# Performance work log

Measured on AMD Instinct MI355X. Metric: run time of the kernel, lower is better.

## Reference

```python
import jax, jax.numpy as jnp
import numpy as np

RADIUS = 0.8
NSAMPLE = 32
EPS = 1e-5  # BatchNorm eps


def _bn(x, gamma, beta, axes):
    # BatchNorm (training-mode batch statistics), channel dim kept via broadcasting
    m = jnp.mean(x, axis=axes, keepdims=True)
    v = jnp.var(x, axis=axes, keepdims=True)
    return (x - m) * jax.lax.rsqrt(v + EPS) * gamma + beta


def setup_inputs() -> dict:
    key = jax.random.key(0)
    ks = jax.random.split(key, 6)
    B, N, P, C, COUT = 4, 8192, 2048, 128, 256
    ffps_xyz = jax.random.uniform(ks[0], (B, P, 3), dtype=jnp.float32) * 2.0 - 1.0
    backbone_xyz = jax.random.uniform(ks[1], (B, N, 3), dtype=jnp.float32) * 2.0 - 1.0
    backbone_features = jax.random.normal(ks[2], (B, C, N), dtype=jnp.float32)
    w_shift = jax.random.normal(ks[3], (3, 3), dtype=jnp.float32) * 0.1
    gamma_shift = jnp.ones((3,), jnp.float32)
    beta_shift = jnp.zeros((3,), jnp.float32)
    w_mlp = jax.random.normal(ks[4], (COUT, 3 + C), dtype=jnp.float32) * 0.05
    gamma_mlp = jnp.ones((COUT,), jnp.float32)
    beta_mlp = jnp.zeros((COUT,), jnp.float32)
    return {
        "ffps_xyz": ffps_xyz,
        "backbone_xyz": backbone_xyz,
        "backbone_features": backbone_features,
        "w_shift": w_shift,
        "gamma_shift": gamma_shift,
        "beta_shift": beta_shift,
        "w_mlp": w_mlp,
        "gamma_mlp": gamma_mlp,
        "beta_mlp": beta_mlp,
    }


def reference(ffps_xyz, backbone_xyz, backbone_features,
              w_shift, gamma_shift, beta_shift,
              w_mlp, gamma_mlp, beta_mlp):
    B, P, _ = ffps_xyz.shape
    N = backbone_xyz.shape[1]

    # ---- shift_layer: Conv1d(3->3, k=1, no bias) + BN1d + ReLU on (B,3,P) ----
    x = jnp.einsum('oc,bpc->bop', w_shift, ffps_xyz)                  # (B,3,P)
    x = _bn(x, gamma_shift[None, :, None], beta_shift[None, :, None], (0, 2))
    new_xyz = jax.nn.relu(x).transpose(0, 2, 1)                       # (B,P,3) query centers

    # ---- QueryAndGroup: ball query (radius, nsample), use_xyz=True ----
    d2 = jnp.sum((new_xyz[:, :, None, :] - backbone_xyz[:, None, :, :]) ** 2, -1)  # (B,P,N)
    within = d2 < (RADIUS * RADIUS)
    # pick the first NSAMPLE in-radius indices (CUDA ball_query semantics)
    keyv = jnp.where(within, jnp.arange(N, dtype=jnp.int32), jnp.int32(N))
    negk, idx = jax.lax.top_k(-keyv, NSAMPLE)                          # smallest keys first
    valid = (-negk) < N
    idx = jnp.where(valid, idx, idx[..., :1])                          # pad with first found idx

    g_xyz = jnp.take_along_axis(backbone_xyz[:, None, :, :], idx[..., None], axis=2)
    g_xyz = g_xyz - new_xyz[:, :, None, :]                             # (B,P,S,3) recentered
    feats = backbone_features.transpose(0, 2, 1)                       # (B,N,C)
    g_f = jnp.take_along_axis(feats[:, None, :, :], idx[..., None], axis=2)  # (B,P,S,C)
    g = jnp.concatenate([g_xyz, g_f], axis=-1)                         # (B,P,S,3+C)

    # ---- mlp: 1x1 conv (3+C -> COUT, no bias) + BN + ReLU ----
    y = jnp.einsum('oc,bpsc->bops', w_mlp, g)                          # (B,COUT,P,S)
    y = _bn(y, gamma_mlp[None, :, None, None], beta_mlp[None, :, None, None], (0, 2, 3))
    y = jax.nn.relu(y)

    # ---- max-pool over neighbor axis, squeeze, transpose ----
    y = jnp.max(y, axis=3)                                             # (B,COUT,P)
    return y.transpose(0, 2, 1)                                        # (B,P,COUT)
```

## Files before the change

kernel.cpp:

```cpp
#include <hip/hip_runtime.h>
#include <math.h>

namespace {
constexpr int B    = 4;
constexpr int N    = 8192;
constexpr int P    = 2048;
constexpr int C    = 128;
constexpr int COUT = 256;
constexpr int NS   = 32;
constexpr int BP   = B * P;
constexpr int BPB  = 2;
constexpr int GRP  = 8;
constexpr int NBLK = BP / (BPB * GRP);

constexpr size_t OFF_FEATT = 0;
constexpr size_t OFF_WSWZ  = 8388608;
constexpr size_t OFF_SSLOT = 8470528;
constexpr size_t OFF_SUMS  = 8471040;
constexpr size_t OFF_IDX   = 8475136;
constexpr size_t OFF_GX    = 9523712;
constexpr size_t OFF_YMAX  = 11620864;
constexpr size_t WS_NEED   = 20009472;
}

typedef short bf16x8 __attribute__((ext_vector_type(8)));
typedef float f32x4  __attribute__((ext_vector_type(4)));

typedef const __attribute__((address_space(1))) void gas_void;
typedef __attribute__((address_space(3))) void las_void;
#define GLOBAL_LOAD_LDS16(gp, lp) \
    __builtin_amdgcn_global_load_lds((gas_void*)(gp), (las_void*)(lp), 16, 0, 0)

__device__ inline unsigned short f2bf(float f) {
    unsigned u = __float_as_uint(f);
    unsigned r = u + 0x7fffu + ((u >> 16) & 1u);
    return (unsigned short)(r >> 16);
}

__global__ __launch_bounds__(256) void k_prep(const float* __restrict__ ffps,
                                              const float* __restrict__ wsh,
                                              double* __restrict__ sslot,
                                              float* __restrict__ sums) {
#pragma clang fp contract(off)
    int blk = blockIdx.x, t = threadIdx.x;
    if (blk == 8) {
        ((f32x4*)sums)[t & 127] = (f32x4){0.f, 0.f, 0.f, 0.f};
        return;
    }
    __shared__ double red[6][256];
    double w[9];
#pragma unroll
    for (int i = 0; i < 9; i++) w[i] = (double)wsh[i];
    double s[3] = {0, 0, 0}, sq[3] = {0, 0, 0};
#pragma unroll
    for (int i = 0; i < 4; i++) {
        int p = blk * 1024 + t + 256 * i;
        double f0 = (double)ffps[p * 3 + 0];
        double f1 = (double)ffps[p * 3 + 1];
        double f2 = (double)ffps[p * 3 + 2];
#pragma unroll
        for (int o = 0; o < 3; o++) {
            double xo = (w[o * 3 + 0] * f0 + w[o * 3 + 1] * f1) + w[o * 3 + 2] * f2;
            s[o] += xo;
            sq[o] += xo * xo;
        }
    }
#pragma unroll
    for (int o = 0; o < 3; o++) { red[o][t] = s[o]; red[3 + o][t] = sq[o]; }
    for (int off = 128; off > 0; off >>= 1) {
        __syncthreads();
        if (t < off) {
#pragma unroll
            for (int j = 0; j < 6; j++) red[j][t] += red[j][t + off];
        }
    }
    __syncthreads();
    if (t < 6) sslot[blk * 6 + t] = red[t][0];
}

__global__ __launch_bounds__(256) void k_front(const float* __restrict__ ffps,
                                               const float* __restrict__ bbxyz,
                                               const float* __restrict__ feat,
                                               const float* __restrict__ wsh,
                                               const float* __restrict__ gsh,
                                               const float* __restrict__ bsh,
                                               const float* __restrict__ wml,
                                               const double* __restrict__ sslot,
                                               unsigned short* __restrict__ featT,
                                               unsigned short* __restrict__ wswz,
                                               int* __restrict__ idxo,
                                               uint2* __restrict__ gxo) {
#pragma clang fp contract(off)
    int blk = blockIdx.x, t = threadIdx.x;
    if (blk >= 2048) {
        int rb = blk - 2048;
        if (rb < 2048) {
            __shared__ float tile[64][33];
            int tx = t & 31, ty = t >> 5;
            int n0 = (rb & 255) * 32, c0 = ((rb >> 8) & 1) * 64, b = rb >> 9;
            const float* src = feat + ((size_t)b * C + c0) * N + n0;
#pragma unroll
            for (int j = 0; j < 8; j++) tile[ty + 8 * j][tx] = src[(size_t)(ty + 8 * j) * N + tx];
            __syncthreads();
            int n = t >> 3;
            int k8 = (t & 7) * 8;
            unsigned vv[4];
#pragma unroll
            for (int i = 0; i < 4; i++) {
                unsigned lo = f2bf(tile[k8 + 2 * i][n]);
                unsigned hi = f2bf(tile[k8 + 2 * i + 1][n]);
                vv[i] = lo | (hi << 16);
            }
            *(int4*)&featT[((size_t)b * N + n0 + n) * C + c0 + k8] =
                make_int4((int)vv[0], (int)vv[1], (int)vv[2], (int)vv[3]);
        } else {
            int i = (rb - 2048) * 256 + t;
            int j = i & 7;
            int lane = (i >> 3) & 63;
            int rest = i >> 9;
            int ks = rest % 5, rt = rest / 5;
            int cout = rt * 16 + (lane & 15);
            int k = ks * 32 + (lane >> 4) * 8 + j;
            float v = 0.f;
            if (k < 128) v = wml[cout * 131 + 3 + k];
            else if (k < 131) v = wml[cout * 131 + (k - 128)];
            wswz[i] = f2bf(v);
        }
        return;
    }

    __shared__ double spar[6];
    if (t < 6) {
        double a = 0.0;
        for (int r = 0; r < 8; r++) a += sslot[r * 6 + t];
        spar[t] = a;
    }
    __syncthreads();
    int wv = t >> 6, lane = t & 63;
    int q = blk * 4 + wv;
    int b = q >> 11;
    double f0 = (double)ffps[q * 3 + 0];
    double f1 = (double)ffps[q * 3 + 1];
    double f2 = (double)ffps[q * 3 + 2];
    double qd[3];
#pragma unroll
    for (int o = 0; o < 3; o++) {
        double m  = spar[o] * (1.0 / 8192.0);
        double v  = spar[3 + o] * (1.0 / 8192.0) - m * m;
        double is = 1.0 / sqrt(v + 1e-5);
        double x  = ((double)wsh[o * 3 + 0] * f0 + (double)wsh[o * 3 + 1] * f1) +
                    (double)wsh[o * 3 + 2] * f2;
        double y  = ((x - m) * is) * (double)gsh[o] + (double)bsh[o];
        qd[o] = (y > 0.0) ? y : 0.0;
    }
    double qx = qd[0], qy = qd[1], qz = qd[2];
    float cfx = (float)qx, cfy = (float)qy, cfz = (float)qz;
    const float* base = bbxyz + (size_t)b * N * 3;
    const double R2 = 0.8 * 0.8;
    {
        double ex = fmax(fmax(qx - 1.0, -1.0 - qx), 0.0);
        double ey = fmax(fmax(qy - 1.0, -1.0 - qy), 0.0);
        double ez = fmax(fmax(qz - 1.0, -1.0 - qz), 0.0);
        if (ex * ex + ey * ey + ez * ez >= R2) {
            if (lane < NS) {
                idxo[q * NS + lane] = 0;
                float rx = base[0] - cfx, ry = base[1] - cfy, rz = base[2] - cfz;
                unsigned u01 = (unsigned)f2bf(rx) | ((unsigned)f2bf(ry) << 16);
                gxo[q * NS + lane] = make_uint2(u01, (unsigned)f2bf(rz));
            }
            return;
        }
    }
    int found = 0, firstn = -1;

    float X0[8], Y0[8], Z0[8], X1[8], Y1[8], Z1[8], X2[8], Y2[8], Z2[8];

    auto loadb = [&](float (&XX)[8], float (&YY)[8], float (&ZZ)[8], int it) {
#pragma unroll
        for (int j = 0; j < 8; j++) {
            int n = it * 512 + j * 64 + lane;
            XX[j] = base[n * 3 + 0];
            YY[j] = base[n * 3 + 1];
            ZZ[j] = base[n * 3 + 2];
        }
    };
    auto proc = [&](float (&XX)[8], float (&YY)[8], float (&ZZ)[8], int it) {
#pragma clang fp contract(off)
#pragma unroll
        for (int j = 0; j < 8; j++) {
            int n = it * 512 + j * 64 + lane;
            double dx = qx - (double)XX[j];
            double dy = qy - (double)YY[j];
            double dz = qz - (double)ZZ[j];
            double d2 = (dx * dx + dy * dy) + dz * dz;
            bool within = d2 < R2;
            unsigned long long mask = __ballot(within);
            if (firstn < 0 && mask != 0ull) firstn = (n - lane) + (__ffsll(mask) - 1);
            if (within) {
                int rank = found + __popcll(mask & ((1ull << lane) - 1ull));
                if (rank < NS) {
                    idxo[q * NS + rank] = n;
                    float rx = XX[j] - cfx, ry = YY[j] - cfy, rz = ZZ[j] - cfz;
                    unsigned u01 = (unsigned)f2bf(rx) | ((unsigned)f2bf(ry) << 16);
                    gxo[q * NS + rank] = make_uint2(u01, (unsigned)f2bf(rz));
                }
            }
            found += __popcll(mask);
        }
    };

    loadb(X0, Y0, Z0, 0);
    loadb(X1, Y1, Z1, 1);
    loadb(X2, Y2, Z2, 2);

    for (int itb = 0; itb < 16; itb += 3) {
        proc(X0, Y0, Z0, itb);
        if (found >= NS) break;
        loadb(X0, Y0, Z0, (itb + 3 < 16) ? itb + 3 : 0);
        if (itb + 1 >= 16) break;
        proc(X1, Y1, Z1, itb + 1);
        if (found >= NS) break;
        loadb(X1, Y1, Z1, (itb + 4 < 16) ? itb + 4 : 0);
        if (itb + 2 >= 16) break;
        proc(X2, Y2, Z2, itb + 2);
        if (found >= NS) break;
        loadb(X2, Y2, Z2, (itb + 5 < 16) ? itb + 5 : 0);
    }
    if (found < NS) {
        int padv = (found == 0) ? 0 : firstn;
        if (lane >= found && lane < NS) {
            idxo[q * NS + lane] = padv;
            float rx = base[padv * 3 + 0] - cfx;
            float ry = base[padv * 3 + 1] - cfy;
            float rz = base[padv * 3 + 2] - cfz;
            unsigned u01 = (unsigned)f2bf(rx) | ((unsigned)f2bf(ry) << 16);
            gxo[q * NS + lane] = make_uint2(u01, (unsigned)f2bf(rz));
        }
    }
}

__global__ __launch_bounds__(256, 2) void k_mlp_mfma(
        const unsigned short* __restrict__ featT,
        const unsigned short* __restrict__ wswz,
        const int* __restrict__ idx,
        const uint2* __restrict__ gxyz,
        float* __restrict__ ymax,
        float* __restrict__ sums) {
    __shared__ alignas(16) unsigned short G[2][4 * 4 * 64 * 8];
    int t = threadIdx.x, lane = t & 63, w = t >> 6;
    int q = lane >> 4, c16 = lane & 15;
    int blk = blockIdx.x;
    int bpbase = blk * (BPB * GRP);
    const bf16x8* wp = (const bf16x8*)wswz;

    bf16x8 wreg[5][4];
#pragma unroll
    for (int ks = 0; ks < 5; ks++)
#pragma unroll
        for (int nt = 0; nt < 4; nt++)
            wreg[ks][nt] = wp[((w * 4 + nt) * 5 + ks) * 64 + lane];

    int sOff = (w >> 1) * NS + (w & 1) * 16 + c16;
    size_t fb = (size_t)(bpbase >> 11) * N * C;

    int nS0 = idx[bpbase * NS + sOff];
    int nS1 = idx[(bpbase + BPB) * NS + sOff];
    uint2 gx_c[4] = {}, gx_n[4] = {};
    if (q == 0)
#pragma unroll
        for (int mt = 0; mt < 4; mt++)
            gx_c[mt] = gxyz[(bpbase + (mt >> 1)) * NS + (mt & 1) * 16 + c16];
    {
        const unsigned short* row = featT + fb + (size_t)nS0 * C + q * 8;
#pragma unroll
        for (int ks = 0; ks < 4; ks++)
            GLOBAL_LOAD_LDS16(row + ks * 32, &G[0][(w * 4 + ks) * 512]);
    }

    float smA[4] = {0.f, 0.f, 0.f, 0.f}, sqA[4] = {0.f, 0.f, 0.f, 0.f};

    for (int g = 0; g < GRP; g++) {
        int buf = g & 1;
        int bp0 = bpbase + g * BPB;
        __syncthreads();
        if (g + 1 < GRP) {
            const unsigned short* row = featT + fb + (size_t)nS1 * C + q * 8;
#pragma unroll
            for (int ks = 0; ks < 4; ks++)
                GLOBAL_LOAD_LDS16(row + ks * 32, &G[buf ^ 1][(w * 4 + ks) * 512]);
            if (q == 0)
#pragma unroll
                for (int mt = 0; mt < 4; mt++)
                    gx_n[mt] = gxyz[(bp0 + BPB + (mt >> 1)) * NS + (mt & 1) * 16 + c16];
        }
        if (g + 2 < GRP) nS0 = idx[(bp0 + 2 * BPB) * NS + sOff];

        f32x4 acc[4][4];
#pragma unroll
        for (int mt = 0; mt < 4; mt++)
#pragma unroll
            for (int nt = 0; nt < 4; nt++) acc[mt][nt] = (f32x4){0.f, 0.f, 0.f, 0.f};

#pragma unroll
        for (int ks = 0; ks < 4; ks++) {
            bf16x8 ag[4];
#pragma unroll
            for (int mt = 0; mt < 4; mt++)
                ag[mt] = *(const bf16x8*)&G[buf][((mt * 4 + ks) * 64 + lane) * 8];
#pragma unroll
            for (int nt = 0; nt < 4; nt++)
#pragma unroll
                for (int mt = 0; mt < 4; mt++)
                    acc[mt][nt] = __builtin_amdgcn_mfma_f32_16x16x32_bf16(ag[mt], wreg[ks][nt], acc[mt][nt], 0, 0, 0);
        }
        {
            bf16x8 agx[4];
#pragma unroll
            for (int mt = 0; mt < 4; mt++) {
                union { int4 i; bf16x8 h; } u;
                u.i = make_int4(q == 0 ? (int)gx_c[mt].x : 0,
                                q == 0 ? (int)gx_c[mt].y : 0, 0, 0);
                agx[mt] = u.h;
            }
#pragma unroll
            for (int nt = 0; nt < 4; nt++)
#pragma unroll
                for (int mt = 0; mt < 4; mt++)
                    acc[mt][nt] = __builtin_amdgcn_mfma_f32_16x16x32_bf16(agx[mt], wreg[4][nt], acc[mt][nt], 0, 0, 0);
        }

#pragma unroll
        for (int pm = 0; pm < BPB; pm++) {
            int bp = bp0 + pm;
#pragma unroll
            for (int nt = 0; nt < 4; nt++) {
                f32x4 a = acc[2 * pm][nt], c = acc[2 * pm + 1][nt];
                float mx = fmaxf(fmaxf(fmaxf(a[0], a[1]), fmaxf(a[2], a[3])),
                                 fmaxf(fmaxf(c[0], c[1]), fmaxf(c[2], c[3])));
                smA[nt] += ((a[0] + a[1]) + (a[2] + a[3])) + ((c[0] + c[1]) + (c[2] + c[3]));
                sqA[nt] += ((a[0] * a[0] + a[1] * a[1]) + (a[2] * a[2] + a[3] * a[3])) +
                           ((c[0] * c[0] + c[1] * c[1]) + (c[2] * c[2] + c[3] * c[3]));
                mx = fmaxf(mx, __shfl_xor(mx, 16, 64));
                mx = fmaxf(mx, __shfl_xor(mx, 32, 64));
                if (q == 0)
                    ymax[(size_t)bp * COUT + w * 64 + nt * 16 + c16] = mx;
            }
        }
        nS1 = nS0;
#pragma unroll
        for (int mt = 0; mt < 4; mt++) gx_c[mt] = gx_n[mt];
    }

#pragma unroll
    for (int nt = 0; nt < 4; nt++) {
        float sm = smA[nt], sq = sqA[nt];
        sm += __shfl_xor(sm, 16, 64);
        sm += __shfl_xor(sm, 32, 64);
        sq += __shfl_xor(sq, 16, 64);
        sq += __shfl_xor(sq, 32, 64);
        if (q == 0) {
            int cout = w * 64 + nt * 16 + c16;
            atomicAdd(&sums[cout], sm);
            atomicAdd(&sums[256 + cout], sq);
        }
    }
}

__global__ __launch_bounds__(256) void k_final(const float* __restrict__ ymax,
                                               const float* __restrict__ sums,
                                               const float* __restrict__ gam,
                                               const float* __restrict__ bet,
                                               float* __restrict__ out) {
    __shared__ float sa[256], sb[256];
    int t = threadIdx.x;
    {
        double sm = (double)sums[t], sq = (double)sums[256 + t];
        double mean = sm * (1.0 / 262144.0);
        double var = sq * (1.0 / 262144.0) - mean * mean;
        double a = (double)gam[t] / sqrt(var + 1e-5);
        sa[t] = (float)a;
        sb[t] = (float)((double)bet[t] - mean * a);
    }
    __syncthreads();
    int i = blockIdx.x * 256 + t;
    int c0 = (t & 63) * 4;
    f32x4 y = *(const f32x4*)&ymax[(size_t)i * 4];
    f32x4 r;
#pragma unroll
    for (int j = 0; j < 4; j++) r[j] = fmaxf(sa[c0 + j] * y[j] + sb[c0 + j], 0.f);
    *(f32x4*)&out[(size_t)i * 4] = r;
}

extern "C" void kernel_launch(void* const* d_in, const int* in_sizes, int n_in,
                              void* d_out, int out_size, void* d_ws, size_t ws_size,
                              hipStream_t stream) {
    const float* ffps  = (const float*)d_in[0];
    const float* bbxyz = (const float*)d_in[1];
    const float* feat  = (const float*)d_in[2];
    const float* wsh   = (const float*)d_in[3];
    const float* gsh   = (const float*)d_in[4];
    const float* bsh   = (const float*)d_in[5];
    const float* wml   = (const float*)d_in[6];
    const float* gml   = (const float*)d_in[7];
    const float* bml   = (const float*)d_in[8];
    float* out = (float*)d_out;
    char* ws = (char*)d_ws;
    if (ws_size < WS_NEED) return;

    unsigned short* featT = (unsigned short*)(ws + OFF_FEATT);
    unsigned short* wswz  = (unsigned short*)(ws + OFF_WSWZ);
    double*         sslot = (double*)(ws + OFF_SSLOT);
    float*          sums  = (float*)(ws + OFF_SUMS);
    int*            idx   = (int*)(ws + OFF_IDX);
    uint2*          gx    = (uint2*)(ws + OFF_GX);
    float*          ymax  = (float*)(ws + OFF_YMAX);

    k_prep<<<dim3(9), dim3(256), 0, stream>>>(ffps, wsh, sslot, sums);
    k_front<<<dim3(2048 + 2048 + 160), dim3(256), 0, stream>>>(
        ffps, bbxyz, feat, wsh, gsh, bsh, wml, sslot, featT, wswz, idx, gx);
    k_mlp_mfma<<<dim3(NBLK), dim3(256), 0, stream>>>(featT, wswz, idx, gx, ymax, sums);
    k_final<<<dim3(BP * COUT / 1024), dim3(256), 0, stream>>>(ymax, sums, gml, bml, out);
}
```

Before: 156.1 us.

## Split MLP output channels across two blocks and use float ball-query distance test

The MLP kernel now launches twice as many blocks, each handling half of the output channels. This halves the weight registers and accumulators per thread and raises the launch-bounds occupancy hint from 2 to 4. The cost is that every gathered feature row is loaded twice, once by each block. The ball query now computes distances in float and falls back to double only when a distance lies within a small margin of the radius, which cuts slow FP64 work. Neighbor indices are also masked with N-1 as a defensive bound.

```diff
diff --git a/kernel.cpp b/kernel.cpp
--- a/kernel.cpp
+++ b/kernel.cpp
@@ -11,7 +11,7 @@
 constexpr int BP   = B * P;
 constexpr int BPB  = 2;
 constexpr int GRP  = 8;
-constexpr int NBLK = BP / (BPB * GRP);
+constexpr int NBLK = (BP / (BPB * GRP)) * 2;
 
 constexpr size_t OFF_FEATT = 0;
 constexpr size_t OFF_WSWZ  = 8388608;
@@ -157,6 +157,7 @@
     float cfx = (float)qx, cfy = (float)qy, cfz = (float)qz;
     const float* base = bbxyz + (size_t)b * N * 3;
     const double R2 = 0.8 * 0.8;
+    const float R2F = 0.64f;
     {
         double ex = fmax(fmax(qx - 1.0, -1.0 - qx), 0.0);
         double ey = fmax(fmax(qy - 1.0, -1.0 - qy), 0.0);
@@ -189,11 +190,19 @@
 #pragma unroll
         for (int j = 0; j < 8; j++) {
             int n = it * 512 + j * 64 + lane;
-            double dx = qx - (double)XX[j];
-            double dy = qy - (double)YY[j];
-            double dz = qz - (double)ZZ[j];
-            double d2 = (dx * dx + dy * dy) + dz * dz;
-            bool within = d2 < R2;
+            float dxf = cfx - XX[j];
+            float dyf = cfy - YY[j];
+            float dzf = cfz - ZZ[j];
+            float d2f = (dxf * dxf + dyf * dyf) + dzf * dzf;
+            bool within;
+            if (__builtin_expect(fabsf(d2f - R2F) < 1e-4f, 0)) {
+                double dx = qx - (double)XX[j];
+                double dy = qy - (double)YY[j];
+                double dz = qz - (double)ZZ[j];
+                within = ((dx * dx + dy * dy) + dz * dz) < R2;
+            } else {
+                within = d2f < R2F;
+            }
             unsigned long long mask = __ballot(within);
             if (firstn < 0 && mask != 0ull) firstn = (n - lane) + (__ffsll(mask) - 1);
             if (within) {
@@ -239,7 +248,7 @@
     }
 }
 
-__global__ __launch_bounds__(256, 2) void k_mlp_mfma(
+__global__ __launch_bounds__(256, 4) void k_mlp_mfma(
         const unsigned short* __restrict__ featT,
         const unsigned short* __restrict__ wswz,
         const int* __restrict__ idx,
@@ -250,21 +259,22 @@
     int t = threadIdx.x, lane = t & 63, w = t >> 6;
     int q = lane >> 4, c16 = lane & 15;
     int blk = blockIdx.x;
-    int bpbase = blk * (BPB * GRP);
+    int nh = blk & 1;
+    int bpbase = (blk >> 1) * (BPB * GRP);
     const bf16x8* wp = (const bf16x8*)wswz;
 
-    bf16x8 wreg[5][4];
+    bf16x8 wreg[5][2];
 #pragma unroll
     for (int ks = 0; ks < 5; ks++)
 #pragma unroll
-        for (int nt = 0; nt < 4; nt++)
-            wreg[ks][nt] = wp[((w * 4 + nt) * 5 + ks) * 64 + lane];
+        for (int nt = 0; nt < 2; nt++)
+            wreg[ks][nt] = wp[((nh * 8 + w * 2 + nt) * 5 + ks) * 64 + lane];
 
     int sOff = (w >> 1) * NS + (w & 1) * 16 + c16;
     size_t fb = (size_t)(bpbase >> 11) * N * C;
 
-    int nS0 = idx[bpbase * NS + sOff];
-    int nS1 = idx[(bpbase + BPB) * NS + sOff];
+    int nS0 = idx[bpbase * NS + sOff] & (N - 1);
+    int nS1 = idx[(bpbase + BPB) * NS + sOff] & (N - 1);
     uint2 gx_c[4] = {}, gx_n[4] = {};
     if (q == 0)
 #pragma unroll
@@ -277,7 +287,7 @@
             GLOBAL_LOAD_LDS16(row + ks * 32, &G[0][(w * 4 + ks) * 512]);
     }
 
-    float smA[4] = {0.f, 0.f, 0.f, 0.f}, sqA[4] = {0.f, 0.f, 0.f, 0.f};
+    float smA[2] = {0.f, 0.f}, sqA[2] = {0.f, 0.f};
 
     for (int g = 0; g < GRP; g++) {
         int buf = g & 1;
@@ -293,13 +303,13 @@
                 for (int mt = 0; mt < 4; mt++)
                     gx_n[mt] = gxyz[(bp0 + BPB + (mt >> 1)) * NS + (mt & 1) * 16 + c16];
         }
-        if (g + 2 < GRP) nS0 = idx[(bp0 + 2 * BPB) * NS + sOff];
-
-        f32x4 acc[4][4];
+        if (g + 2 < GRP) nS0 = idx[(bp0 + 2 * BPB) * NS + sOff] & (N - 1);
+
+        f32x4 acc[4][2];
 #pragma unroll
         for (int mt = 0; mt < 4; mt++)
 #pragma unroll
-            for (int nt = 0; nt < 4; nt++) acc[mt][nt] = (f32x4){0.f, 0.f, 0.f, 0.f};
+            for (int nt = 0; nt < 2; nt++) acc[mt][nt] = (f32x4){0.f, 0.f, 0.f, 0.f};
 
 #pragma unroll
         for (int ks = 0; ks < 4; ks++) {
@@ -308,7 +318,7 @@
             for (int mt = 0; mt < 4; mt++)
                 ag[mt] = *(const bf16x8*)&G[buf][((mt * 4 + ks) * 64 + lane) * 8];
 #pragma unroll
-            for (int nt = 0; nt < 4; nt++)
+            for (int nt = 0; nt < 2; nt++)
 #pragma unroll
                 for (int mt = 0; mt < 4; mt++)
                     acc[mt][nt] = __builtin_amdgcn_mfma_f32_16x16x32_bf16(ag[mt], wreg[ks][nt], acc[mt][nt], 0, 0, 0);
@@ -323,7 +333,7 @@
                 agx[mt] = u.h;
             }
 #pragma unroll
-            for (int nt = 0; nt < 4; nt++)
+            for (int nt = 0; nt < 2; nt++)
 #pragma unroll
                 for (int mt = 0; mt < 4; mt++)
                     acc[mt][nt] = __builtin_amdgcn_mfma_f32_16x16x32_bf16(agx[mt], wreg[4][nt], acc[mt][nt], 0, 0, 0);
@@ -333,7 +343,7 @@
         for (int pm = 0; pm < BPB; pm++) {
             int bp = bp0 + pm;
 #pragma unroll
-            for (int nt = 0; nt < 4; nt++) {
+            for (int nt = 0; nt < 2; nt++) {
                 f32x4 a = acc[2 * pm][nt], c = acc[2 * pm + 1][nt];
                 float mx = fmaxf(fmaxf(fmaxf(a[0], a[1]), fmaxf(a[2], a[3])),
                                  fmaxf(fmaxf(c[0], c[1]), fmaxf(c[2], c[3])));
@@ -343,7 +353,7 @@
                 mx = fmaxf(mx, __shfl_xor(mx, 16, 64));
                 mx = fmaxf(mx, __shfl_xor(mx, 32, 64));
                 if (q == 0)
-                    ymax[(size_t)bp * COUT + w * 64 + nt * 16 + c16] = mx;
+                    ymax[(size_t)bp * COUT + nh * 128 + w * 32 + nt * 16 + c16] = mx;
             }
         }
         nS1 = nS0;
@@ -352,14 +362,14 @@
     }
 
 #pragma unroll
-    for (int nt = 0; nt < 4; nt++) {
+    for (int nt = 0; nt < 2; nt++) {
         float sm = smA[nt], sq = sqA[nt];
         sm += __shfl_xor(sm, 16, 64);
         sm += __shfl_xor(sm, 32, 64);
         sq += __shfl_xor(sq, 16, 64);
         sq += __shfl_xor(sq, 32, 64);
         if (q == 0) {
-            int cout = w * 64 + nt * 16 + c16;
+            int cout = nh * 128 + w * 32 + nt * 16 + c16;
             atomicAdd(&sums[cout], sm);
             atomicAdd(&sums[256 + cout], sq);
         }
```

Result: no change. 155.5 us (-0.4%).

## Fuse ball query into MFMA MLP kernel and merge prep work into one launch

Applied to the files above, without the earlier changes.

Moves the ball-query search into the MLP kernel so neighbor indices and recentered xyz stay in shared memory instead of round-tripping through global workspace. The feature transpose and weight swizzle move into the prep kernel, cutting the launch count from four to three. The distance test now runs in float and falls back to double only near the radius boundary. Each block now handles 8 query points rather than 16, and the serial ball-query phase inside the MLP block may reduce overlap and occupancy.

```diff
diff --git a/kernel.cpp b/kernel.cpp
--- a/kernel.cpp
+++ b/kernel.cpp
@@ -9,18 +9,15 @@
 constexpr int COUT = 256;
 constexpr int NS   = 32;
 constexpr int BP   = B * P;
-constexpr int BPB  = 2;
-constexpr int GRP  = 8;
-constexpr int NBLK = BP / (BPB * GRP);
+constexpr int BPK  = 8;
+constexpr int NBLK = BP / BPK;
 
 constexpr size_t OFF_FEATT = 0;
 constexpr size_t OFF_WSWZ  = 8388608;
 constexpr size_t OFF_SSLOT = 8470528;
 constexpr size_t OFF_SUMS  = 8471040;
-constexpr size_t OFF_IDX   = 8475136;
-constexpr size_t OFF_GX    = 9523712;
-constexpr size_t OFF_YMAX  = 11620864;
-constexpr size_t WS_NEED   = 20009472;
+constexpr size_t OFF_YMAX  = 8475136;
+constexpr size_t WS_NEED   = 16863744;
 }
 
 typedef short bf16x8 __attribute__((ext_vector_type(8)));
@@ -37,331 +34,330 @@
     return (unsigned short)(r >> 16);
 }
 
+
 __global__ __launch_bounds__(256) void k_prep(const float* __restrict__ ffps,
                                               const float* __restrict__ wsh,
+                                              const float* __restrict__ feat,
+                                              const float* __restrict__ wml,
                                               double* __restrict__ sslot,
-                                              float* __restrict__ sums) {
+                                              float* __restrict__ sums,
+                                              unsigned short* __restrict__ featT,
+                                              unsigned short* __restrict__ wswz) {
 #pragma clang fp contract(off)
     int blk = blockIdx.x, t = threadIdx.x;
-    if (blk == 8) {
-        ((f32x4*)sums)[t & 127] = (f32x4){0.f, 0.f, 0.f, 0.f};
-        return;
+    if (blk < 8) {
+        __shared__ double red[6][256];
+        double w[9];
+#pragma unroll
+        for (int i = 0; i < 9; i++) w[i] = (double)wsh[i];
+        double s[3] = {0, 0, 0}, sq[3] = {0, 0, 0};
+#pragma unroll
+        for (int i = 0; i < 4; i++) {
+            int p = blk * 1024 + t + 256 * i;
+            double f0 = (double)ffps[p * 3 + 0];
+            double f1 = (double)ffps[p * 3 + 1];
+            double f2 = (double)ffps[p * 3 + 2];
+#pragma unroll
+            for (int o = 0; o < 3; o++) {
+                double xo = (w[o * 3 + 0] * f0 + w[o * 3 + 1] * f1) + w[o * 3 + 2] * f2;
+                s[o] += xo;
+                sq[o] += xo * xo;
+            }
+        }
+#pragma unroll
+        for (int o = 0; o < 3; o++) { red[o][t] = s[o]; red[3 + o][t] = sq[o]; }
+        for (int off = 128; off > 0; off >>= 1) {
+            __syncthreads();
+            if (t < off) {
+#pragma unroll
+                for (int j = 0; j < 6; j++) red[j][t] += red[j][t + off];
+            }
+        }
+        __syncthreads();
+        if (t < 6) sslot[blk * 6 + t] = red[t][0];
+    } else if (blk == 8) {
+        if (t < 128) ((f32x4*)sums)[t] = (f32x4){0.f, 0.f, 0.f, 0.f};
+    } else if (blk < 2057) {
+        __shared__ float tile[64][33];
+        int rb = blk - 9;
+        int tx = t & 31, ty = t >> 5;
+        int n0 = (rb & 255) * 32, c0 = ((rb >> 8) & 1) * 64, b = rb >> 9;
+        const float* src = feat + ((size_t)b * C + c0) * N + n0;
+#pragma unroll
+        for (int j = 0; j < 8; j++) tile[ty + 8 * j][tx] = src[(size_t)(ty + 8 * j) * N + tx];
+        __syncthreads();
+        int n = t >> 3;
+        int k8 = (t & 7) * 8;
+        unsigned vv[4];
+#pragma unroll
+        for (int i = 0; i < 4; i++) {
+            unsigned lo = f2bf(tile[k8 + 2 * i][n]);
+            unsigned hi = f2bf(tile[k8 + 2 * i + 1][n]);
+            vv[i] = lo | (hi << 16);
+        }
+        *(int4*)&featT[((size_t)b * N + n0 + n) * C + c0 + k8] =
+            make_int4((int)vv[0], (int)vv[1], (int)vv[2], (int)vv[3]);
+    } else {
+        int i = (blk - 2057) * 256 + t;
+        int j = i & 7;
+        int lane = (i >> 3) & 63;
+        int rest = i >> 9;
+        int ks = rest % 5, rt = rest / 5;
+        int cout = rt * 16 + (lane & 15);
+        int k = ks * 32 + (lane >> 4) * 8 + j;
+        float v = 0.f;
+        if (k < 128) v = wml[cout * 131 + 3 + k];
+        else if (k < 131) v = wml[cout * 131 + (k - 128)];
+        wswz[i] = f2bf(v);
     }
-    __shared__ double red[6][256];
-    double w[9];
-#pragma unroll
-    for (int i = 0; i < 9; i++) w[i] = (double)wsh[i];
-    double s[3] = {0, 0, 0}, sq[3] = {0, 0, 0};
-#pragma unroll
-    for (int i = 0; i < 4; i++) {
-        int p = blk * 1024 + t + 256 * i;
-        double f0 = (double)ffps[p * 3 + 0];
-        double f1 = (double)ffps[p * 3 + 1];
-        double f2 = (double)ffps[p * 3 + 2];
-#pragma unroll
-        for (int o = 0; o < 3; o++) {
-            double xo = (w[o * 3 + 0] * f0 + w[o * 3 + 1] * f1) + w[o * 3 + 2] * f2;
-            s[o] += xo;
-            sq[o] += xo * xo;
-        }
-    }
-#pragma unroll
-    for (int o = 0; o < 3; o++) { red[o][t] = s[o]; red[3 + o][t] = sq[o]; }
-    for (int off = 128; off > 0; off >>= 1) {
-        __syncthreads();
-        if (t < off) {
-#pragma unroll
-            for (int j = 0; j < 6; j++) red[j][t] += red[j][t + off];
-        }
-    }
-    __syncthreads();
-    if (t < 6) sslot[blk * 6 + t] = red[t][0];
-}
-
-__global__ __launch_bounds__(256) void k_front(const float* __restrict__ ffps,
-                                               const float* __restrict__ bbxyz,
-                                               const float* __restrict__ feat,
-                                               const float* __restrict__ wsh,
-                                               const float* __restrict__ gsh,
-                                               const float* __restrict__ bsh,
-                                               const float* __restrict__ wml,
-                                               const double* __restrict__ sslot,
-                                               unsigned short* __restrict__ featT,
-                                               unsigned short* __restrict__ wswz,
-                                               int* __restrict__ idxo,
-                                               uint2* __restrict__ gxo) {
+}
+
+__global__ __launch_bounds__(256, 2) void k_fused(
+        const float* __restrict__ ffps,
+        const float* __restrict__ bbxyz,
+        const float* __restrict__ wsh,
+        const float* __restrict__ gsh,
+        const float* __restrict__ bsh,
+        const unsigned short* __restrict__ featT,
+        const unsigned short* __restrict__ wswz,
+        const double* __restrict__ sslot,
+        float* __restrict__ ymax,
+        float* __restrict__ sums) {
 #pragma clang fp contract(off)
-    int blk = blockIdx.x, t = threadIdx.x;
-    if (blk >= 2048) {
-        int rb = blk - 2048;
-        if (rb < 2048) {
-            __shared__ float tile[64][33];
-            int tx = t & 31, ty = t >> 5;
-            int n0 = (rb & 255) * 32, c0 = ((rb >> 8) & 1) * 64, b = rb >> 9;
-            const float* src = feat + ((size_t)b * C + c0) * N + n0;
-#pragma unroll
-            for (int j = 0; j < 8; j++) tile[ty + 8 * j][tx] = src[(size_t)(ty + 8 * j) * N + tx];
-            __syncthreads();
-            int n = t >> 3;
-            int k8 = (t & 7) * 8;
-            unsigned vv[4];
-#pragma unroll
-            for (int i = 0; i < 4; i++) {
-                unsigned lo = f2bf(tile[k8 + 2 * i][n]);
-                unsigned hi = f2bf(tile[k8 + 2 * i + 1][n]);
-                vv[i] = lo | (hi << 16);
-            }
-            *(int4*)&featT[((size_t)b * N + n0 + n) * C + c0 + k8] =
-                make_int4((int)vv[0], (int)vv[1], (int)vv[2], (int)vv[3]);
-        } else {
-            int i = (rb - 2048) * 256 + t;
-            int j = i & 7;
-            int lane = (i >> 3) & 63;
-            int rest = i >> 9;
-            int ks = rest % 5, rt = rest / 5;
-            int cout = rt * 16 + (lane & 15);
-            int k = ks * 32 + (lane >> 4) * 8 + j;
-            float v = 0.f;
-            if (k < 128) v = wml[cout * 131 + 3 + k];
-            else if (k < 131) v = wml[cout * 131 + (k - 128)];
-            wswz[i] = f2bf(v);
-        }
-        return;
-    }
-
+    __shared__ alignas(16) unsigned short G[2][4 * 4 * 64 * 8];
+    __shared__ int idxs[BPK][NS];
+    __shared__ uint2 gxs[BPK][NS];
     __shared__ double spar[6];
+    int t = threadIdx.x, lane = t & 63, wv = t >> 6;
+    int blk = blockIdx.x;
+    int bp0 = blk * BPK;
+
     if (t < 6) {
         double a = 0.0;
         for (int r = 0; r < 8; r++) a += sslot[r * 6 + t];
         spar[t] = a;
     }
     __syncthreads();
-    int wv = t >> 6, lane = t & 63;
-    int q = blk * 4 + wv;
-    int b = q >> 11;
-    double f0 = (double)ffps[q * 3 + 0];
-    double f1 = (double)ffps[q * 3 + 1];
-    double f2 = (double)ffps[q * 3 + 2];
-    double qd[3];
-#pragma unroll
-    for (int o = 0; o < 3; o++) {
-        double m  = spar[o] * (1.0 / 8192.0);
-        double v  = spar[3 + o] * (1.0 / 8192.0) - m * m;
-        double is = 1.0 / sqrt(v + 1e-5);
-        double x  = ((double)wsh[o * 3 + 0] * f0 + (double)wsh[o * 3 + 1] * f1) +
-                    (double)wsh[o * 3 + 2] * f2;
-        double y  = ((x - m) * is) * (double)gsh[o] + (double)bsh[o];
-        qd[o] = (y > 0.0) ? y : 0.0;
+
+    for (int qi = 0; qi < 2; qi++) {
+        int lq = wv * 2 + qi;
+        int q = bp0 + lq;
+        double f0 = (double)ffps[q * 3 + 0];
+        double f1 = (double)ffps[q * 3 + 1];
+        double f2 = (double)ffps[q * 3 + 2];
+        double qd[3];
+#pragma unroll
+        for (int o = 0; o < 3; o++) {
+            double m  = spar[o] * (1.0 / 8192.0);
+            double v  = spar[3 + o] * (1.0 / 8192.0) - m * m;
+            double is = 1.0 / sqrt(v + 1e-5);
+            double x  = ((double)wsh[o * 3 + 0] * f0 + (double)wsh[o * 3 + 1] * f1) +
+                        (double)wsh[o * 3 + 2] * f2;
+            double y  = ((x - m) * is) * (double)gsh[o] + (double)bsh[o];
+            qd[o] = (y > 0.0) ? y : 0.0;
+        }
+        double qx = qd[0], qy = qd[1], qz = qd[2];
+        float cfx = (float)qx, cfy = (float)qy, cfz = (float)qz;
+        const float* base = bbxyz + (size_t)(q >> 11) * N * 3;
+        const double R2 = 0.8 * 0.8;
+        const float R2F = 0.64f;
+        {
+            double ex = fmax(fmax(qx - 1.0, -1.0 - qx), 0.0);
+            double ey = fmax(fmax(qy - 1.0, -1.0 - qy), 0.0);
+            double ez = fmax(fmax(qz - 1.0, -1.0 - qz), 0.0);
+            if (ex * ex + ey * ey + ez * ez >= R2) {
+                if (lane < NS) {
+                    idxs[lq][lane] = 0;
+                    float rx = base[0] - cfx, ry = base[1] - cfy, rz = base[2] - cfz;
+                    unsigned u01 = (unsigned)f2bf(rx) | ((unsigned)f2bf(ry) << 16);
+                    gxs[lq][lane] = make_uint2(u01, (unsigned)f2bf(rz));
+                }
+                continue;
+            }
+        }
+        int found = 0, firstn = -1;
+
+        float X0[8], Y0[8], Z0[8], X1[8], Y1[8], Z1[8], X2[8], Y2[8], Z2[8];
+
+        auto loadb = [&](float (&XX)[8], float (&YY)[8], float (&ZZ)[8], int it) {
+#pragma unroll
+            for (int j = 0; j < 8; j++) {
+                int n = it * 512 + j * 64 + lane;
+                XX[j] = base[n * 3 + 0];
+                YY[j] = base[n * 3 + 1];
+                ZZ[j] = base[n * 3 + 2];
+            }
+        };
+        auto proc = [&](float (&XX)[8], float (&YY)[8], float (&ZZ)[8], int it) {
+#pragma clang fp contract(off)
+#pragma unroll
+            for (int j = 0; j < 8; j++) {
+                int n = it * 512 + j * 64 + lane;
+                float dxf = cfx - XX[j];
+                float dyf = cfy - YY[j];
+                float dzf = cfz - ZZ[j];
+                float d2f = (dxf * dxf + dyf * dyf) + dzf * dzf;
+                bool within;
+                if (__builtin_expect(fabsf(d2f - R2F) < 1e-4f, 0)) {
+                    double dx = qx - (double)XX[j];
+                    double dy = qy - (double)YY[j];
+                    double dz = qz - (double)ZZ[j];
+                    within = ((dx * dx + dy * dy) + dz * dz) < R2;
+                } else {
+                    within = d2f < R2F;
+                }
+                unsigned long long mask = __ballot(within);
+                if (firstn < 0 && mask != 0ull) firstn = (n - lane) + (__ffsll(mask) - 1);
+                if (within) {
+                    int rank = found + __popcll(mask & ((1ull << lane) - 1ull));
+                    if (rank < NS) {
+                        idxs[lq][rank] = n;
+                        float rx = XX[j] - cfx, ry = YY[j] - cfy, rz = ZZ[j] - cfz;
+                        unsigned u01 = (unsigned)f2bf(rx) | ((unsigned)f2bf(ry) << 16);
+                        gxs[lq][rank] = make_uint2(u01, (unsigned)f2bf(rz));
+                    }
+                }
+                found += __popcll(mask);
+            }
+        };
+
+        loadb(X0, Y0, Z0, 0);
+        loadb(X1, Y1, Z1, 1);
+        loadb(X2, Y2, Z2, 2);
+
+        for (int itb = 0; itb < 16; itb += 3) {
+            proc(X0, Y0, Z0, itb);
+            if (found >= NS) break;
+            loadb(X0, Y0, Z0, (itb + 3 < 16) ? itb + 3 : 0);
+            if (itb + 1 >= 16) break;
+            proc(X1, Y1, Z1, itb + 1);
+            if (found >= NS) break;
+            loadb(X1, Y1, Z1, (itb + 4 < 16) ? itb + 4 : 0);
+            if (itb + 2 >= 16) break;
+            proc(X2, Y2, Z2, itb + 2);
+            if (found >= NS) break;
+            loadb(X2, Y2, Z2, (itb + 5 < 16) ? itb + 5 : 0);
+        }
+        if (found < NS) {
+            int padv = (found == 0) ? 0 : firstn;
+            if (lane >= found && lane < NS) {
+                idxs[lq][lane] = padv;
+                float rx = base[padv * 3 + 0] - cfx;
+                float ry = base[padv * 3 + 1] - cfy;
+                float rz = base[padv * 3 + 2] - cfz;
+                unsigned u01 = (unsigned)f2bf(rx) | ((unsigned)f2bf(ry) << 16);
+                gxs[lq][lane] = make_uint2(u01, (unsigned)f2bf(rz));
+            }
+        }
     }
-    double qx = qd[0], qy = qd[1], qz = qd[2];
-    float cfx = (float)qx, cfy = (float)qy, cfz = (float)qz;
-    const float* base = bbxyz + (size_t)b * N * 3;
-    const double R2 = 0.8 * 0.8;
+    __syncthreads();
+
     {
-        double ex = fmax(fmax(qx - 1.0, -1.0 - qx), 0.0);
-        double ey = fmax(fmax(qy - 1.0, -1.0 - qy), 0.0);
-        double ez = fmax(fmax(qz - 1.0, -1.0 - qz), 0.0);
-        if (ex * ex + ey * ey + ez * ez >= R2) {
-            if (lane < NS) {
-                idxo[q * NS + lane] = 0;
-                float rx = base[0] - cfx, ry = base[1] - cfy, rz = base[2] - cfz;
-                unsigned u01 = (unsigned)f2bf(rx) | ((unsigned)f2bf(ry) << 16);
-                gxo[q * NS + lane] = make_uint2(u01, (unsigned)f2bf(rz));
-            }
-            return;
-        }
-    }
-    int found = 0, firstn = -1;
-
-    float X0[8], Y0[8], Z0[8], X1[8], Y1[8], Z1[8], X2[8], Y2[8], Z2[8];
-
-    auto loadb = [&](float (&XX)[8], float (&YY)[8], float (&ZZ)[8], int it) {
-#pragma unroll
-        for (int j = 0; j < 8; j++) {
-            int n = it * 512 + j * 64 + lane;
-            XX[j] = base[n * 3 + 0];
-            YY[j] = base[n * 3 + 1];
-            ZZ[j] = base[n * 3 + 2];
-        }
-    };
-    auto proc = [&](float (&XX)[8], float (&YY)[8], float (&ZZ)[8], int it) {
-#pragma clang fp contract(off)
-#pragma unroll
-        for (int j = 0; j < 8; j++) {
-            int n = it * 512 + j * 64 + lane;
-            double dx = qx - (double)XX[j];
-            double dy = qy - (double)YY[j];
-            double dz = qz - (double)ZZ[j];
-            double d2 = (dx * dx + dy * dy) + dz * dz;
-            bool within = d2 < R2;
-            unsigned long long mask = __ballot(within);
-            if (firstn < 0 && mask != 0ull) firstn = (n - lane) + (__ffsll(mask) - 1);
-            if (within) {
-                int rank = found + __popcll(mask & ((1ull << lane) - 1ull));
-                if (rank < NS) {
-                    idxo[q * NS + rank] = n;
-                    float rx = XX[j] - cfx, ry = YY[j] - cfy, rz = ZZ[j] - cfz;
-                    unsigned u01 = (unsigned)f2bf(rx) | ((unsigned)f2bf(ry) << 16);
-                    gxo[q * NS + rank] = make_uint2(u01, (unsigned)f2bf(rz));
+        int w = wv;
+        int qq = lane >> 4, c16 = lane & 15;
+        const bf16x8* wp = (const bf16x8*)wswz;
+        size_t fb = (size_t)(bp0 >> 11) * N * C;
+
+        bf16x8 wreg[5][4];
+#pragma unroll
+        for (int ks = 0; ks < 5; ks++)
+#pragma unroll
+            for (int nt = 0; nt < 4; nt++)
+                wreg[ks][nt] = wp[((w * 4 + nt) * 5 + ks) * 64 + lane];
+
+        {
+            int n0 = idxs[(w >> 1)][(w & 1) * 16 + c16];
+            const unsigned short* row = featT + fb + (size_t)n0 * C + qq * 8;
+#pragma unroll
+            for (int ks = 0; ks < 4; ks++)
+                GLOBAL_LOAD_LDS16(row + ks * 32, &G[0][(w * 4 + ks) * 512]);
+        }
+
+        float smA[4] = {0.f, 0.f, 0.f, 0.f}, sqA[4] = {0.f, 0.f, 0.f, 0.f};
+
+        for (int g = 0; g < 4; g++) {
+            int buf = g & 1;
+            __syncthreads();
+            if (g + 1 < 4) {
+                int n1 = idxs[(g + 1) * 2 + (w >> 1)][(w & 1) * 16 + c16];
+                const unsigned short* row = featT + fb + (size_t)n1 * C + qq * 8;
+#pragma unroll
+                for (int ks = 0; ks < 4; ks++)
+                    GLOBAL_LOAD_LDS16(row + ks * 32, &G[buf ^ 1][(w * 4 + ks) * 512]);
+            }
+
+            f32x4 acc[4][4];
+#pragma unroll
+            for (int mt = 0; mt < 4; mt++)
+#pragma unroll
+                for (int nt = 0; nt < 4; nt++) acc[mt][nt] = (f32x4){0.f, 0.f, 0.f, 0.f};
+
+#pragma unroll
+            for (int ks = 0; ks < 4; ks++) {
+                bf16x8 ag[4];
+#pragma unroll
+                for (int mt = 0; mt < 4; mt++)
+                    ag[mt] = *(const bf16x8*)&G[buf][((mt * 4 + ks) * 64 + lane) * 8];
+#pragma unroll
+                for (int nt = 0; nt < 4; nt++)
+#pragma unroll
+                    for (int mt = 0; mt < 4; mt++)
+                        acc[mt][nt] = __builtin_amdgcn_mfma_f32_16x16x32_bf16(
+                            ag[mt], wreg[ks][nt], acc[mt][nt], 0, 0, 0);
+            }
+            {
+                bf16x8 agx[4];
+#pragma unroll
+                for (int mt = 0; mt < 4; mt++) {
+                    unsigned u01 = 0, u23 = 0;
+                    if (qq == 0) {
+                        uint2 gv = gxs[g * 2 + (mt >> 1)][(mt & 1) * 16 + c16];
+                        u01 = gv.x;
+                        u23 = gv.y;
+                    }
+                    union { int4 i; bf16x8 h; } u;
+                    u.i = make_int4((int)u01, (int)u23, 0, 0);
+                    agx[mt] = u.h;
                 }
-            }
-            found += __popcll(mask);
-        }
-    };
-
-    loadb(X0, Y0, Z0, 0);
-    loadb(X1, Y1, Z1, 1);
-    loadb(X2, Y2, Z2, 2);
-
-    for (int itb = 0; itb < 16; itb += 3) {
-        proc(X0, Y0, Z0, itb);
-        if (found >= NS) break;
-        loadb(X0, Y0, Z0, (itb + 3 < 16) ? itb + 3 : 0);
-        if (itb + 1 >= 16) break;
-        proc(X1, Y1, Z1, itb + 1);
-        if (found >= NS) break;
-        loadb(X1, Y1, Z1, (itb + 4 < 16) ? itb + 4 : 0);
-        if (itb + 2 >= 16) break;
-        proc(X2, Y2, Z2, itb + 2);
-        if (found >= NS) break;
-        loadb(X2, Y2, Z2, (itb + 5 < 16) ? itb + 5 : 0);
-    }
-    if (found < NS) {
-        int padv = (found == 0) ? 0 : firstn;
-        if (lane >= found && lane < NS) {
-            idxo[q * NS + lane] = padv;
-            float rx = base[padv * 3 + 0] - cfx;
-            float ry = base[padv * 3 + 1] - cfy;
-            float rz = base[padv * 3 + 2] - cfz;
-            unsigned u01 = (unsigned)f2bf(rx) | ((unsigned)f2bf(ry) << 16);
-            gxo[q * NS + lane] = make_uint2(u01, (unsigned)f2bf(rz));
-        }
-    }
-}
-
-__global__ __launch_bounds__(256, 2) void k_mlp_mfma(
-        const unsigned short* __restrict__ featT,
-        const unsigned short* __restrict__ wswz,
-        const int* __restrict__ idx,
-        const uint2* __restrict__ gxyz,
-        float* __restrict__ ymax,
-        float* __restrict__ sums) {
-    __shared__ alignas(16) unsigned short G[2][4 * 4 * 64 * 8];
-    int t = threadIdx.x, lane = t & 63, w = t >> 6;
-    int q = lane >> 4, c16 = lane & 15;
-    int blk = blockIdx.x;
-    int bpbase = blk * (BPB * GRP);
-    const bf16x8* wp = (const bf16x8*)wswz;
-
-    bf16x8 wreg[5][4];
-#pragma unroll
-    for (int ks = 0; ks < 5; ks++)
-#pragma unroll
-        for (int nt = 0; nt < 4; nt++)
-            wreg[ks][nt] = wp[((w * 4 + nt) * 5 + ks) * 64 + lane];
-
-    int sOff = (w >> 1) * NS + (w & 1) * 16 + c16;
-    size_t fb = (size_t)(bpbase >> 11) * N * C;
-
-    int nS0 = idx[bpbase * NS + sOff];
-    int nS1 = idx[(bpbase + BPB) * NS + sOff];
-    uint2 gx_c[4] = {}, gx_n[4] = {};
-    if (q == 0)
-#pragma unroll
-        for (int mt = 0; mt < 4; mt++)
-            gx_c[mt] = gxyz[(bpbase + (mt >> 1)) * NS + (mt & 1) * 16 + c16];
-    {
-        const unsigned short* row = featT + fb + (size_t)nS0 * C + q * 8;
-#pragma unroll
-        for (int ks = 0; ks < 4; ks++)
-            GLOBAL_LOAD_LDS16(row + ks * 32, &G[0][(w * 4 + ks) * 512]);
-    }
-
-    float smA[4] = {0.f, 0.f, 0.f, 0.f}, sqA[4] = {0.f, 0.f, 0.f, 0.f};
-
-    for (int g = 0; g < GRP; g++) {
-        int buf = g & 1;
-        int bp0 = bpbase + g * BPB;
-        __syncthreads();
-        if (g + 1 < GRP) {
-            const unsigned short* row = featT + fb + (size_t)nS1 * C + q * 8;
-#pragma unroll
-            for (int ks = 0; ks < 4; ks++)
-                GLOBAL_LOAD_LDS16(row + ks * 32, &G[buf ^ 1][(w * 4 + ks) * 512]);
-            if (q == 0)
-#pragma unroll
-                for (int mt = 0; mt < 4; mt++)
-                    gx_n[mt] = gxyz[(bp0 + BPB + (mt >> 1)) * NS + (mt & 1) * 16 + c16];
-        }
-        if (g + 2 < GRP) nS0 = idx[(bp0 + 2 * BPB) * NS + sOff];
-
-        f32x4 acc[4][4];
-#pragma unroll
-        for (int mt = 0; mt < 4; mt++)
-#pragma unroll
-            for (int nt = 0; nt < 4; nt++) acc[mt][nt] = (f32x4){0.f, 0.f, 0.f, 0.f};
-
-#pragma unroll
-        for (int ks = 0; ks < 4; ks++) {
-            bf16x8 ag[4];
-#pragma unroll
-            for (int mt = 0; mt < 4; mt++)
-                ag[mt] = *(const bf16x8*)&G[buf][((mt * 4 + ks) * 64 + lane) * 8];
-#pragma unroll
-            for (int nt = 0; nt < 4; nt++)
-#pragma unroll
-                for (int mt = 0; mt < 4; mt++)
-                    acc[mt][nt] = __builtin_amdgcn_mfma_f32_16x16x32_bf16(ag[mt], wreg[ks][nt], acc[mt][nt], 0, 0, 0);
-        }
-        {
-            bf16x8 agx[4];
-#pragma unroll
-            for (int mt = 0; mt < 4; mt++) {
-                union { int4 i; bf16x8 h; } u;
-                u.i = make_int4(q == 0 ? (int)gx_c[mt].x : 0,
-                                q == 0 ? (int)gx_c[mt].y : 0, 0, 0);
-                agx[mt] = u.h;
-            }
-#pragma unroll
-            for (int nt = 0; nt < 4; nt++)
-#pragma unroll
-                for (int mt = 0; mt < 4; mt++)
-                    acc[mt][nt] = __builtin_amdgcn_mfma_f32_16x16x32_bf16(agx[mt], wreg[4][nt], acc[mt][nt], 0, 0, 0);
-        }
-
-#pragma unroll
-        for (int pm = 0; pm < BPB; pm++) {
-            int bp = bp0 + pm;
-#pragma unroll
-            for (int nt = 0; nt < 4; nt++) {
-                f32x4 a = acc[2 * pm][nt], c = acc[2 * pm + 1][nt];
-                float mx = fmaxf(fmaxf(fmaxf(a[0], a[1]), fmaxf(a[2], a[3])),
-                                 fmaxf(fmaxf(c[0], c[1]), fmaxf(c[2], c[3])));
-                smA[nt] += ((a[0] + a[1]) + (a[2] + a[3])) + ((c[0] + c[1]) + (c[2] + c[3]));
-                sqA[nt] += ((a[0] * a[0] + a[1] * a[1]) + (a[2] * a[2] + a[3] * a[3])) +
-                           ((c[0] * c[0] + c[1] * c[1]) + (c[2] * c[2] + c[3] * c[3]));
-                mx = fmaxf(mx, __shfl_xor(mx, 16, 64));
-                mx = fmaxf(mx, __shfl_xor(mx, 32, 64));
-                if (q == 0)
-                    ymax[(size_t)bp * COUT + w * 64 + nt * 16 + c16] = mx;
-            }
-        }
-        nS1 = nS0;
-#pragma unroll
-        for (int mt = 0; mt < 4; mt++) gx_c[mt] = gx_n[mt];
-    }
-
-#pragma unroll
-    for (int nt = 0; nt < 4; nt++) {
-        float sm = smA[nt], sq = sqA[nt];
-        sm += __shfl_xor(sm, 16, 64);
-        sm += __shfl_xor(sm, 32, 64);
-        sq += __shfl_xor(sq, 16, 64);
-        sq += __shfl_xor(sq, 32, 64);
-        if (q == 0) {
-            int cout = w * 64 + nt * 16 + c16;
-            atomicAdd(&sums[cout], sm);
-            atomicAdd(&sums[256 + cout], sq);
+#pragma unroll
+                for (int nt = 0; nt < 4; nt++)
+#pragma unroll
+                    for (int mt = 0; mt < 4; mt++)
+                        acc[mt][nt] = __builtin_amdgcn_mfma_f32_16x16x32_bf16(
+                            agx[mt], wreg[4][nt], acc[mt][nt], 0, 0, 0);
+            }
+
+#pragma unroll
+            for (int pm = 0; pm < 2; pm++) {
+                int bp = bp0 + g * 2 + pm;
+#pragma unroll
+                for (int nt = 0; nt < 4; nt++) {
+                    f32x4 a = acc[2 * pm][nt], c = acc[2 * pm + 1][nt];
+                    float mx = fmaxf(fmaxf(fmaxf(a[0], a[1]), fmaxf(a[2], a[3])),
+                                     fmaxf(fmaxf(c[0], c[1]), fmaxf(c[2], c[3])));
+                    smA[nt] += ((a[0] + a[1]) + (a[2] + a[3])) + ((c[0] + c[1]) + (c[2] + c[3]));
+                    sqA[nt] += ((a[0] * a[0] + a[1] * a[1]) + (a[2] * a[2] + a[3] * a[3])) +
+                               ((c[0] * c[0] + c[1] * c[1]) + (c[2] * c[2] + c[3] * c[3]));
+                    mx = fmaxf(mx, __shfl_xor(mx, 16, 64));
+                    mx = fmaxf(mx, __shfl_xor(mx, 32, 64));
+                    if (qq == 0)
+                        ymax[(size_t)bp * COUT + w * 64 + nt * 16 + c16] = mx;
+                }
+            }
+        }
+
+#pragma unroll
+        for (int nt = 0; nt < 4; nt++) {
+            float sm = smA[nt], sq = sqA[nt];
+            sm += __shfl_xor(sm, 16, 64);
+            sm += __shfl_xor(sm, 32, 64);
+            sq += __shfl_xor(sq, 16, 64);
+            sq += __shfl_xor(sq, 32, 64);
+            if (qq == 0) {
+                int cout = w * 64 + nt * 16 + c16;
+                atomicAdd(&sums[cout], sm);
+                atomicAdd(&sums[256 + cout], sq);
+            }
         }
     }
 }
@@ -411,13 +407,11 @@
     unsigned short* wswz  = (unsigned short*)(ws + OFF_WSWZ);
     double*         sslot = (double*)(ws + OFF_SSLOT);
     float*          sums  = (float*)(ws + OFF_SUMS);
-    int*            idx   = (int*)(ws + OFF_IDX);
-    uint2*          gx    = (uint2*)(ws + OFF_GX);
     float*          ymax  = (float*)(ws + OFF_YMAX);
 
-    k_prep<<<dim3(9), dim3(256), 0, stream>>>(ffps, wsh, sslot, sums);
-    k_front<<<dim3(2048 + 2048 + 160), dim3(256), 0, stream>>>(
-        ffps, bbxyz, feat, wsh, gsh, bsh, wml, sslot, featT, wswz, idx, gx);
-    k_mlp_mfma<<<dim3(NBLK), dim3(256), 0, stream>>>(featT, wswz, idx, gx, ymax, sums);
+    k_prep<<<dim3(2217), dim3(256), 0, stream>>>(ffps, wsh, feat, wml,
+                                                 sslot, sums, featT, wswz);
+    k_fused<<<dim3(NBLK), dim3(256), 0, stream>>>(ffps, bbxyz, wsh, gsh, bsh,
+                                                  featT, wswz, sslot, ymax, sums);
     k_final<<<dim3(BP * COUT / 1024), dim3(256), 0, stream>>>(ymax, sums, gml, bml, out);
 }
```

Measured after the change: 181.0 us. 1.16x slower.
